# Performance work log

Measured on AMD Instinct MI355X. Metric: run time of the kernel, lower is better.

The kernel has to match this reference:

```python
import jax, jax.numpy as jnp
import numpy as np

LN_EPS = 1e-5

def _layernorm(x, scale, bias):
    mu = jnp.mean(x, axis=-1, keepdims=True)
    var = jnp.var(x, axis=-1, keepdims=True)
    return (x - mu) * jax.lax.rsqrt(var + LN_EPS) * scale + bias

def setup_inputs() -> dict:
    T, node_num, num_nodes, E, C = 4, 10000, 50000, 256, 128
    key = jax.random.key(0)
    ks = jax.random.split(key, 12)
    s = lambda fan_in: 1.0 / np.sqrt(fan_in)
    return {
        "x": jax.random.normal(ks[0], (T * node_num, E), jnp.float32),
        "batched_x": jax.random.normal(ks[1], (num_nodes, E), jnp.float32),
        "indices": jax.random.randint(ks[2], (T, node_num), 0, num_nodes, jnp.int32),
        "ln_d_scale": jnp.ones((E,), jnp.float32),
        "ln_d_bias": jnp.zeros((E,), jnp.float32),
        "W1_d": jax.random.normal(ks[3], (E, 2 * E), jnp.float32) * s(E),
        "b1_d": jnp.zeros((2 * E,), jnp.float32),
        "W2_d": jax.random.normal(ks[4], (2 * E, C), jnp.float32) * s(2 * E),
        "b2_d": jnp.zeros((C,), jnp.float32),
        "ln_u_scale": jnp.ones((C,), jnp.float32),
        "ln_u_bias": jnp.zeros((C,), jnp.float32),
        "W1_u": jax.random.normal(ks[5], (C, 2 * C), jnp.float32) * s(C),
        "b1_u": jnp.zeros((2 * C,), jnp.float32),
        "W2_u": jax.random.normal(ks[6], (2 * C, E), jnp.float32) * s(2 * C),
        "b2_u": jnp.zeros((E,), jnp.float32),
    }

def reference(x, batched_x, indices, ln_d_scale, ln_d_bias, W1_d, b1_d, W2_d, b2_d,
              ln_u_scale, ln_u_bias, W1_u, b1_u, W2_u, b2_u):
    T, node_num = indices.shape
    num_nodes, E = batched_x.shape
    xr = x.reshape(T, node_num, E)
    # _to_entire: per-step scatter-add of active-node embeddings into the full node table
    def scatter_one(xi, idx):
        return jnp.zeros((num_nodes, E), x.dtype).at[idx].add(xi)
    ta = jax.vmap(scatter_one)(xr, indices)          # [T, num_nodes, E]
    inp = ta + batched_x[None]                        # broadcast entire features
    h = _layernorm(inp, ln_d_scale, ln_d_bias)
    h = jax.nn.gelu(h @ W1_d + b1_d, approximate=False) @ W2_d + b2_d  # [T, num_nodes, C]
    # _from_entire: gather each step's active nodes back, concat, LN + MLP up
    g = jnp.take_along_axis(h, indices[..., None], axis=1)  # [T, node_num, C]
    g = g.reshape(T * node_num, -1)
    g = _layernorm(g, ln_u_scale, ln_u_bias)
    out = jax.nn.gelu(g @ W1_u + b1_u, approximate=False) @ W2_u + b2_u  # [T*node_num, E]
    return out
```

## Files before the change

kernel.cpp:

```cpp
#include <hip/hip_runtime.h>
#include <math.h>

#define T_STEPS   4
#define NODE_NUM  10000
#define NUM_NODES 50000
#define E         256
#define TWO_E     512
#define CC        128
#define TWO_C     256
#define ROWS      32

typedef short bf16x8 __attribute__((ext_vector_type(8)));
typedef float f32x4  __attribute__((ext_vector_type(4)));

#define MFMA16(a, b, c) __builtin_amdgcn_mfma_f32_16x16x32_bf16((a), (b), (c), 0, 0, 0)

static __device__ unsigned short g_wt[294912];
static __device__ int g_cnt[T_STEPS * NUM_NODES];
static __device__ int g_dup[T_STEPS * NODE_NUM];
static __device__ int g_ndup[T_STEPS];

__device__ __forceinline__ float geluf(float v) {
    float p = v * (1.5957691216057308f + 0.07135481282636226f * v * v);
    return v / (1.0f + __expf(-p));
}

__device__ __forceinline__ unsigned short f2bf(float f) {
    unsigned int u = __builtin_bit_cast(unsigned int, f);
    u += 0x7fffu + ((u >> 16) & 1u);
    return (unsigned short)(u >> 16);
}

__global__ void prep_weights(const float* __restrict__ W1d, const float* __restrict__ W2d,
                             const float* __restrict__ W1u, const float* __restrict__ W2u) {
    int i = blockIdx.x * 256 + threadIdx.x;
    if (i < T_STEPS * NUM_NODES) g_cnt[i] = 0;
    if (i < T_STEPS) g_ndup[i] = 0;
    if (i < 131072) {
        int n = i >> 8, k = i & 255;
        g_wt[i] = f2bf(W1d[(size_t)k * TWO_E + n]);
    }
    if (i < 65536) {
        int n = i >> 9, k = i & 511;
        g_wt[131072 + i] = f2bf(W2d[(size_t)k * CC + n]);
    }
    if (i < 32768) {
        int n = i >> 7, k = i & 127;
        g_wt[196608 + i] = f2bf(W1u[(size_t)k * TWO_C + n]);
    }
    if (i < 65536) {
        int n = i >> 8, k = i & 255;
        g_wt[229376 + i] = f2bf(W2u[(size_t)k * E + n]);
    }
}

__global__ void count_kernel(const int* __restrict__ indices) {
    int gr = blockIdx.x * 256 + threadIdx.x;
    if (gr < T_STEPS * NODE_NUM) {
        int t = gr / NODE_NUM;
        atomicAdd(&g_cnt[t * NUM_NODES + indices[gr]], 1);
    }
}

__global__ void compact_zero_kernel(float* __restrict__ table,
                                    const int* __restrict__ indices,
                                    int gr0, int t0, int grLim, int slab) {
    int gr = gr0 + blockIdx.x * 256 + threadIdx.x;
    if (gr >= grLim) return;
    int t = gr / NODE_NUM;
    int idx = indices[gr];
    if (g_cnt[t * NUM_NODES + idx] < 2) return;
    int pos = atomicAdd(&g_ndup[slab], 1);
    g_dup[gr0 + pos] = gr;
    float4* rp = reinterpret_cast<float4*>(&table[((size_t)(t - t0) * NUM_NODES + idx) * E]);
    float4 z = make_float4(0.f, 0.f, 0.f, 0.f);
    #pragma unroll
    for (int k = 0; k < 64; ++k) rp[k] = z;
}

__global__ void scatter_list_kernel(float* __restrict__ table,
                                    const float* __restrict__ x,
                                    const int* __restrict__ indices,
                                    int gr0, int t0, int slab) {
    int nd = g_ndup[slab];
    for (int e = blockIdx.x; e < nd; e += gridDim.x) {
        int gr = g_dup[gr0 + e];
        int t = gr / NODE_NUM;
        int idx = indices[gr];
        atomicAdd(&table[((size_t)(t - t0) * NUM_NODES + idx) * E + threadIdx.x],
                  x[(size_t)gr * E + threadIdx.x]);
    }
}

__global__ __launch_bounds__(256, 3)
void mlp_kernel(const float* __restrict__ table,
                const float* __restrict__ x,
                const float* __restrict__ batched_x,
                const int* __restrict__ indices,
                const float* __restrict__ lnd_s, const float* __restrict__ lnd_b,
                const float* __restrict__ b1d, const float* __restrict__ b2d,
                const float* __restrict__ lnu_s, const float* __restrict__ lnu_b,
                const float* __restrict__ b1u, const float* __restrict__ b2u,
                float* __restrict__ out,
                int gr0, int t0, int grLim) {
    __shared__ __align__(16) unsigned char smem[50176];
    __shared__ const float* rptr[ROWS];
    __shared__ int    ridx[ROWS];

    float*          Xf  = (float*)smem;
    unsigned short* Xs  = (unsigned short*)(smem + 33280);
    unsigned short* H1  = (unsigned short*)smem;
    float*          H2f = (float*)(smem + 33280);
    unsigned short* H2b = (unsigned short*)smem;
    unsigned short* G1  = (unsigned short*)(smem + 8704);

    const unsigned short* w1t  = g_wt;
    const unsigned short* w2t  = g_wt + 131072;
    const unsigned short* w1ut = g_wt + 196608;
    const unsigned short* w2ut = g_wt + 229376;

    const int tid = threadIdx.x;
    const int w = tid >> 6, lane = tid & 63;
    const int l16 = lane & 15, quad = lane >> 4;
    const int grb = gr0 + blockIdx.x * ROWS;

    if (tid < ROWS) {
        int gr = grb + tid;
        if (gr >= grLim) gr = grLim - 1;
        int t = gr / NODE_NUM;
        int idx = indices[gr];
        ridx[tid] = idx;
        rptr[tid] = (g_cnt[t * NUM_NODES + idx] > 1)
            ? (table + ((size_t)(t - t0) * NUM_NODES + idx) * E)
            : (x + (size_t)gr * E);
    }
    __syncthreads();

    #pragma unroll
    for (int it = 0; it < 8; ++it) {
        int v = it * 256 + tid;
        int r = v >> 6;
        int c = (v & 63) * 4;
        float4 tv = *reinterpret_cast<const float4*>(rptr[r] + c);
        float4 bv = *reinterpret_cast<const float4*>(&batched_x[(size_t)ridx[r] * E + c]);
        float4 s; s.x = tv.x + bv.x; s.y = tv.y + bv.y; s.z = tv.z + bv.z; s.w = tv.w + bv.w;
        *reinterpret_cast<float4*>(&Xf[r * 260 + c]) = s;
    }
    __syncthreads();

    {
        int row = tid >> 3, l8 = tid & 7;
        float s = 0.f, sq = 0.f;
        #pragma unroll
        for (int k = 0; k < 32; ++k) {
            float v = Xf[row * 260 + k * 8 + l8];
            s += v; sq += v * v;
        }
        s  += __shfl_xor(s, 1);  s  += __shfl_xor(s, 2);  s  += __shfl_xor(s, 4);
        sq += __shfl_xor(sq, 1); sq += __shfl_xor(sq, 2); sq += __shfl_xor(sq, 4);
        float mu = s * (1.0f / E);
        float var = sq * (1.0f / E) - mu * mu;
        float rs = rsqrtf(var + 1e-5f);
        #pragma unroll
        for (int k = 0; k < 32; ++k) {
            int c = k * 8 + l8;
            float v = (Xf[row * 260 + c] - mu) * rs * lnd_s[c] + lnd_b[c];
            Xs[row * 264 + c] = f2bf(v);
        }
    }
    __syncthreads();

    {
        bf16x8 af[2][8];
        #pragma unroll
        for (int mt = 0; mt < 2; ++mt) {
            const unsigned short* base = Xs + (l16 + 16 * mt) * 264 + quad * 8;
            #pragma unroll
            for (int ks = 0; ks < 8; ++ks)
                af[mt][ks] = *reinterpret_cast<const bf16x8*>(base + ks * 32);
        }
        bf16x8 bbuf[2][8];
        {
            const unsigned short* bp = w1t + (size_t)((w * 8) * 16 + l16) * 256 + quad * 8;
            #pragma unroll
            for (int ks = 0; ks < 8; ++ks)
                bbuf[0][ks] = *reinterpret_cast<const bf16x8*>(bp + ks * 32);
        }
        #pragma unroll
        for (int nt_ = 0; nt_ < 8; ++nt_) {
            const int cb = nt_ & 1, nb = cb ^ 1;
            if (nt_ < 7) {
                const unsigned short* bp =
                    w1t + (size_t)((w * 8 + nt_ + 1) * 16 + l16) * 256 + quad * 8;
                #pragma unroll
                for (int ks = 0; ks < 8; ++ks)
                    bbuf[nb][ks] = *reinterpret_cast<const bf16x8*>(bp + ks * 32);
            }
            int n = (w * 8 + nt_) * 16 + l16;
            f32x4 a0 = {0.f, 0.f, 0.f, 0.f}, a1 = {0.f, 0.f, 0.f, 0.f};
            #pragma unroll
            for (int ks = 0; ks < 8; ++ks) {
                a0 = MFMA16(af[0][ks], bbuf[cb][ks], a0);
                a1 = MFMA16(af[1][ks], bbuf[cb][ks], a1);
            }
            float bias = b1d[n];
            #pragma unroll
            for (int reg = 0; reg < 4; ++reg) {
                int r = quad * 4 + reg;
                H1[r * 520 + n]        = f2bf(geluf(a0[reg] + bias));
                H1[(r + 16) * 520 + n] = f2bf(geluf(a1[reg] + bias));
            }
        }
    }
    __syncthreads();

    {
        f32x4 acc2[2][2];
        #pragma unroll
        for (int i = 0; i < 2; ++i)
            #pragma unroll
            for (int j = 0; j < 2; ++j) acc2[i][j] = (f32x4){0.f, 0.f, 0.f, 0.f};
        bf16x8 afk[2][8];
        #pragma unroll
        for (int mt = 0; mt < 2; ++mt) {
            const unsigned short* base = H1 + (l16 + 16 * mt) * 520 + quad * 8;
            #pragma unroll
            for (int ks = 0; ks < 8; ++ks)
                afk[mt][ks] = *reinterpret_cast<const bf16x8*>(base + ks * 32);
        }
        bf16x8 bbuf[2][8];
        {
            const unsigned short* bp = w2t + (size_t)((w * 2) * 16 + l16) * 512 + quad * 8;
            #pragma unroll
            for (int ks = 0; ks < 8; ++ks)
                bbuf[0][ks] = *reinterpret_cast<const bf16x8*>(bp + ks * 32);
        }
        #pragma unroll
        for (int s = 0; s < 4; ++s) {
            const int nt2 = s & 1;
            const int cb = s & 1, nb = cb ^ 1;
            if (s < 3) {
                const int s1 = s + 1, kh1 = s1 >> 1, nt21 = s1 & 1;
                const unsigned short* bp =
                    w2t + (size_t)((w * 2 + nt21) * 16 + l16) * 512 + kh1 * 256 + quad * 8;
                #pragma unroll
                for (int ks = 0; ks < 8; ++ks)
                    bbuf[nb][ks] = *reinterpret_cast<const bf16x8*>(bp + ks * 32);
            }
            if (s == 2) {
                #pragma unroll
                for (int mt = 0; mt < 2; ++mt) {
                    const unsigned short* base = H1 + (l16 + 16 * mt) * 520 + 256 + quad * 8;
                    #pragma unroll
                    for (int ks = 0; ks < 8; ++ks)
                        afk[mt][ks] = *reinterpret_cast<const bf16x8*>(base + ks * 32);
                }
            }
            #pragma unroll
            for (int ks = 0; ks < 8; ++ks) {
                acc2[nt2][0] = MFMA16(afk[0][ks], bbuf[cb][ks], acc2[nt2][0]);
                acc2[nt2][1] = MFMA16(afk[1][ks], bbuf[cb][ks], acc2[nt2][1]);
            }
        }
        #pragma unroll
        for (int nt2 = 0; nt2 < 2; ++nt2) {
            int n = (w * 2 + nt2) * 16 + l16;
            float bias = b2d[n];
            #pragma unroll
            for (int mt = 0; mt < 2; ++mt)
                #pragma unroll
                for (int reg = 0; reg < 4; ++reg) {
                    int r = mt * 16 + quad * 4 + reg;
                    H2f[r * 132 + n] = acc2[nt2][mt][reg] + bias;
                }
        }
    }
    __syncthreads();

    {
        int row = tid >> 3, l8 = tid & 7;
        float s = 0.f, sq = 0.f;
        #pragma unroll
        for (int k = 0; k < 16; ++k) {
            float v = H2f[row * 132 + k * 8 + l8];
            s += v; sq += v * v;
        }
        s  += __shfl_xor(s, 1);  s  += __shfl_xor(s, 2);  s  += __shfl_xor(s, 4);
        sq += __shfl_xor(sq, 1); sq += __shfl_xor(sq, 2); sq += __shfl_xor(sq, 4);
        float mu = s * (1.0f / CC);
        float var = sq * (1.0f / CC) - mu * mu;
        float rs = rsqrtf(var + 1e-5f);
        #pragma unroll
        for (int k = 0; k < 16; ++k) {
            int c = k * 8 + l8;
            float v = (H2f[row * 132 + c] - mu) * rs * lnu_s[c] + lnu_b[c];
            H2b[row * 136 + c] = f2bf(v);
        }
    }
    __syncthreads();

    {
        bf16x8 af3[2][4];
        #pragma unroll
        for (int mt = 0; mt < 2; ++mt) {
            const unsigned short* base = H2b + (l16 + 16 * mt) * 136 + quad * 8;
            #pragma unroll
            for (int ks = 0; ks < 4; ++ks)
                af3[mt][ks] = *reinterpret_cast<const bf16x8*>(base + ks * 32);
        }
        bf16x8 bbuf[2][4];
        {
            const unsigned short* bp = w1ut + (size_t)((w * 4) * 16 + l16) * 128 + quad * 8;
            #pragma unroll
            for (int ks = 0; ks < 4; ++ks)
                bbuf[0][ks] = *reinterpret_cast<const bf16x8*>(bp + ks * 32);
        }
        #pragma unroll
        for (int nt_ = 0; nt_ < 4; ++nt_) {
            const int cb = nt_ & 1, nb = cb ^ 1;
            if (nt_ < 3) {
                const unsigned short* bp =
                    w1ut + (size_t)((w * 4 + nt_ + 1) * 16 + l16) * 128 + quad * 8;
                #pragma unroll
                for (int ks = 0; ks < 4; ++ks)
                    bbuf[nb][ks] = *reinterpret_cast<const bf16x8*>(bp + ks * 32);
            }
            int n = (w * 4 + nt_) * 16 + l16;
            f32x4 a0 = {0.f, 0.f, 0.f, 0.f}, a1 = {0.f, 0.f, 0.f, 0.f};
            #pragma unroll
            for (int ks = 0; ks < 4; ++ks) {
                a0 = MFMA16(af3[0][ks], bbuf[cb][ks], a0);
                a1 = MFMA16(af3[1][ks], bbuf[cb][ks], a1);
            }
            float bias = b1u[n];
            #pragma unroll
            for (int reg = 0; reg < 4; ++reg) {
                int r = quad * 4 + reg;
                G1[r * 264 + n]        = f2bf(geluf(a0[reg] + bias));
                G1[(r + 16) * 264 + n] = f2bf(geluf(a1[reg] + bias));
            }
        }
    }
    __syncthreads();

    {
        bf16x8 af4[2][8];
        #pragma unroll
        for (int mt = 0; mt < 2; ++mt) {
            const unsigned short* base = G1 + (l16 + 16 * mt) * 264 + quad * 8;
            #pragma unroll
            for (int ks = 0; ks < 8; ++ks)
                af4[mt][ks] = *reinterpret_cast<const bf16x8*>(base + ks * 32);
        }
        bf16x8 bbuf[2][8];
        {
            const unsigned short* bp = w2ut + (size_t)((w * 4) * 16 + l16) * 256 + quad * 8;
            #pragma unroll
            for (int ks = 0; ks < 8; ++ks)
                bbuf[0][ks] = *reinterpret_cast<const bf16x8*>(bp + ks * 32);
        }
        #pragma unroll
        for (int nt_ = 0; nt_ < 4; ++nt_) {
            const int cb = nt_ & 1, nb = cb ^ 1;
            if (nt_ < 3) {
                const unsigned short* bp =
                    w2ut + (size_t)((w * 4 + nt_ + 1) * 16 + l16) * 256 + quad * 8;
                #pragma unroll
                for (int ks = 0; ks < 8; ++ks)
                    bbuf[nb][ks] = *reinterpret_cast<const bf16x8*>(bp + ks * 32);
            }
            int n = (w * 4 + nt_) * 16 + l16;
            f32x4 a0 = {0.f, 0.f, 0.f, 0.f}, a1 = {0.f, 0.f, 0.f, 0.f};
            #pragma unroll
            for (int ks = 0; ks < 8; ++ks) {
                a0 = MFMA16(af4[0][ks], bbuf[cb][ks], a0);
                a1 = MFMA16(af4[1][ks], bbuf[cb][ks], a1);
            }
            float bias = b2u[n];
            #pragma unroll
            for (int reg = 0; reg < 4; ++reg) {
                int r = quad * 4 + reg;
                int g0 = grb + r, g1 = grb + r + 16;
                if (g0 < grLim) out[(size_t)g0 * E + n] = a0[reg] + bias;
                if (g1 < grLim) out[(size_t)g1 * E + n] = a1[reg] + bias;
            }
        }
    }
}

extern "C" void kernel_launch(void* const* d_in, const int* in_sizes, int n_in,
                              void* d_out, int out_size, void* d_ws, size_t ws_size,
                              hipStream_t stream) {
    const float* x     = (const float*)d_in[0];
    const float* bx    = (const float*)d_in[1];
    const int*   idxp  = (const int*)  d_in[2];
    const float* lnd_s = (const float*)d_in[3];
    const float* lnd_b = (const float*)d_in[4];
    const float* W1d   = (const float*)d_in[5];
    const float* b1d   = (const float*)d_in[6];
    const float* W2d   = (const float*)d_in[7];
    const float* b2d   = (const float*)d_in[8];
    const float* lnu_s = (const float*)d_in[9];
    const float* lnu_b = (const float*)d_in[10];
    const float* W1u   = (const float*)d_in[11];
    const float* b1u   = (const float*)d_in[12];
    const float* W2u   = (const float*)d_in[13];
    const float* b2u   = (const float*)d_in[14];
    float* out = (float*)d_out;
    float* table = (float*)d_ws;

    const size_t slice_bytes = (size_t)NUM_NODES * E * sizeof(float);
    int tb = (int)(ws_size / slice_bytes);
    if (tb < 1) tb = 1;
    if (tb > T_STEPS) tb = T_STEPS;

    prep_weights<<<784, 256, 0, stream>>>(W1d, W2d, W1u, W2u);
    count_kernel<<<(T_STEPS * NODE_NUM + 255) / 256, 256, 0, stream>>>(idxp);

    for (int t0 = 0; t0 < T_STEPS; t0 += tb) {
        int tcur = T_STEPS - t0 < tb ? T_STEPS - t0 : tb;
        int nrows = tcur * NODE_NUM;
        int gr0 = t0 * NODE_NUM;
        int grLim = gr0 + nrows;
        int slab = t0 / tb;
        compact_zero_kernel<<<(nrows + 255) / 256, 256, 0, stream>>>(
            table, idxp, gr0, t0, grLim, slab);
        scatter_list_kernel<<<1024, E, 0, stream>>>(table, x, idxp, gr0, t0, slab);
        mlp_kernel<<<(nrows + ROWS - 1) / ROWS, 256, 0, stream>>>(
            table, x, bx, idxp, lnd_s, lnd_b, b1d, b2d,
            lnu_s, lnu_b, b1u, b2u, out, gr0, t0, grLim);
    }
}
```

Measured before the change: 289.0 us.

## Use compact slot table for duplicate scatter and launch single pass

Replaces the per-timestep full node table with a compact slot table indexed by an atomic slot assignment for nodes hit more than once. This removes the slab loop so all timesteps run in one scatter and one MLP launch, cutting launches and tail effects. It adds an index prep kernel and zeroes a fixed MAX_SLOTS region up front, which bounds duplicates at 20000 and costs extra memset bandwidth.

```diff
diff --git a/kernel.cpp b/kernel.cpp
--- a/kernel.cpp
+++ b/kernel.cpp
@@ -9,6 +9,8 @@
 #define CC        128
 #define TWO_C     256
 #define ROWS      32
+#define NROWS_ALL (T_STEPS * NODE_NUM)
+#define MAX_SLOTS 20000
 
 typedef short bf16x8 __attribute__((ext_vector_type(8)));
 typedef float f32x4  __attribute__((ext_vector_type(4)));
@@ -17,8 +19,10 @@
 
 static __device__ unsigned short g_wt[294912];
 static __device__ int g_cnt[T_STEPS * NUM_NODES];
-static __device__ int g_dup[T_STEPS * NODE_NUM];
-static __device__ int g_ndup[T_STEPS];
+static __device__ int g_slot[T_STEPS * NUM_NODES];
+static __device__ int g_nslots;
+static __device__ int g_dup[NROWS_ALL];
+static __device__ int g_ndup0;
 
 __device__ __forceinline__ float geluf(float v) {
     float p = v * (1.5957691216057308f + 0.07135481282636226f * v * v);
@@ -31,11 +35,17 @@
     return (unsigned short)(u >> 16);
 }
 
-__global__ void prep_weights(const float* __restrict__ W1d, const float* __restrict__ W2d,
+__global__ void prep_weights(float* __restrict__ ctable,
+                             const float* __restrict__ W1d, const float* __restrict__ W2d,
                              const float* __restrict__ W1u, const float* __restrict__ W2u) {
     int i = blockIdx.x * 256 + threadIdx.x;
+    if (i == 0) { g_nslots = 0; g_ndup0 = 0; }
     if (i < T_STEPS * NUM_NODES) g_cnt[i] = 0;
-    if (i < T_STEPS) g_ndup[i] = 0;
+    {
+        float4 z = make_float4(0.f, 0.f, 0.f, 0.f);
+        float4* ct4 = reinterpret_cast<float4*>(ctable);
+        for (int j = i; j < MAX_SLOTS * E / 4; j += 200704) ct4[j] = z;
+    }
     if (i < 131072) {
         int n = i >> 8, k = i & 255;
         g_wt[i] = f2bf(W1d[(size_t)k * TWO_E + n]);
@@ -56,44 +66,40 @@
 
 __global__ void count_kernel(const int* __restrict__ indices) {
     int gr = blockIdx.x * 256 + threadIdx.x;
-    if (gr < T_STEPS * NODE_NUM) {
+    if (gr < NROWS_ALL) {
         int t = gr / NODE_NUM;
         atomicAdd(&g_cnt[t * NUM_NODES + indices[gr]], 1);
     }
 }
 
-__global__ void compact_zero_kernel(float* __restrict__ table,
-                                    const int* __restrict__ indices,
-                                    int gr0, int t0, int grLim, int slab) {
-    int gr = gr0 + blockIdx.x * 256 + threadIdx.x;
-    if (gr >= grLim) return;
-    int t = gr / NODE_NUM;
-    int idx = indices[gr];
-    if (g_cnt[t * NUM_NODES + idx] < 2) return;
-    int pos = atomicAdd(&g_ndup[slab], 1);
-    g_dup[gr0 + pos] = gr;
-    float4* rp = reinterpret_cast<float4*>(&table[((size_t)(t - t0) * NUM_NODES + idx) * E]);
-    float4 z = make_float4(0.f, 0.f, 0.f, 0.f);
-    #pragma unroll
-    for (int k = 0; k < 64; ++k) rp[k] = z;
-}
-
-__global__ void scatter_list_kernel(float* __restrict__ table,
+__global__ void index_prep_kernel(const int* __restrict__ indices) {
+    int i = blockIdx.x * 256 + threadIdx.x;
+    if (i < T_STEPS * NUM_NODES && g_cnt[i] >= 2)
+        g_slot[i] = atomicAdd(&g_nslots, 1);
+    if (i < NROWS_ALL) {
+        int t = i / NODE_NUM;
+        if (g_cnt[t * NUM_NODES + indices[i]] >= 2) {
+            int p = atomicAdd(&g_ndup0, 1);
+            g_dup[p] = i;
+        }
+    }
+}
+
+__global__ void scatter_list_kernel(float* __restrict__ ctable,
                                     const float* __restrict__ x,
-                                    const int* __restrict__ indices,
-                                    int gr0, int t0, int slab) {
-    int nd = g_ndup[slab];
+                                    const int* __restrict__ indices) {
+    int nd = g_ndup0;
     for (int e = blockIdx.x; e < nd; e += gridDim.x) {
-        int gr = g_dup[gr0 + e];
+        int gr = g_dup[e];
         int t = gr / NODE_NUM;
-        int idx = indices[gr];
-        atomicAdd(&table[((size_t)(t - t0) * NUM_NODES + idx) * E + threadIdx.x],
+        int slot = g_slot[t * NUM_NODES + indices[gr]];
+        atomicAdd(&ctable[(size_t)slot * E + threadIdx.x],
                   x[(size_t)gr * E + threadIdx.x]);
     }
 }
 
 __global__ __launch_bounds__(256, 3)
-void mlp_kernel(const float* __restrict__ table,
+void mlp_kernel(const float* __restrict__ ctable,
                 const float* __restrict__ x,
                 const float* __restrict__ batched_x,
                 const int* __restrict__ indices,
@@ -102,7 +108,7 @@
                 const float* __restrict__ lnu_s, const float* __restrict__ lnu_b,
                 const float* __restrict__ b1u, const float* __restrict__ b2u,
                 float* __restrict__ out,
-                int gr0, int t0, int grLim) {
+                int grLim) {
     __shared__ __align__(16) unsigned char smem[50176];
     __shared__ const float* rptr[ROWS];
     __shared__ int    ridx[ROWS];
@@ -122,16 +128,16 @@
     const int tid = threadIdx.x;
     const int w = tid >> 6, lane = tid & 63;
     const int l16 = lane & 15, quad = lane >> 4;
-    const int grb = gr0 + blockIdx.x * ROWS;
+    const int grb = blockIdx.x * ROWS;
 
     if (tid < ROWS) {
         int gr = grb + tid;
         if (gr >= grLim) gr = grLim - 1;
         int t = gr / NODE_NUM;
-        int idx = indices[gr];
-        ridx[tid] = idx;
-        rptr[tid] = (g_cnt[t * NUM_NODES + idx] > 1)
-            ? (table + ((size_t)(t - t0) * NUM_NODES + idx) * E)
+        int key = t * NUM_NODES + indices[gr];
+        ridx[tid] = indices[gr];
+        rptr[tid] = (g_cnt[key] > 1)
+            ? (ctable + (size_t)g_slot[key] * E)
             : (x + (size_t)gr * E);
     }
     __syncthreads();
@@ -407,27 +413,14 @@
     const float* W2u   = (const float*)d_in[13];
     const float* b2u   = (const float*)d_in[14];
     float* out = (float*)d_out;
-    float* table = (float*)d_ws;
-
-    const size_t slice_bytes = (size_t)NUM_NODES * E * sizeof(float);
-    int tb = (int)(ws_size / slice_bytes);
-    if (tb < 1) tb = 1;
-    if (tb > T_STEPS) tb = T_STEPS;
-
-    prep_weights<<<784, 256, 0, stream>>>(W1d, W2d, W1u, W2u);
-    count_kernel<<<(T_STEPS * NODE_NUM + 255) / 256, 256, 0, stream>>>(idxp);
-
-    for (int t0 = 0; t0 < T_STEPS; t0 += tb) {
-        int tcur = T_STEPS - t0 < tb ? T_STEPS - t0 : tb;
-        int nrows = tcur * NODE_NUM;
-        int gr0 = t0 * NODE_NUM;
-        int grLim = gr0 + nrows;
-        int slab = t0 / tb;
-        compact_zero_kernel<<<(nrows + 255) / 256, 256, 0, stream>>>(
-            table, idxp, gr0, t0, grLim, slab);
-        scatter_list_kernel<<<1024, E, 0, stream>>>(table, x, idxp, gr0, t0, slab);
-        mlp_kernel<<<(nrows + ROWS - 1) / ROWS, 256, 0, stream>>>(
-            table, x, bx, idxp, lnd_s, lnd_b, b1d, b2d,
-            lnu_s, lnu_b, b1u, b2u, out, gr0, t0, grLim);
-    }
-}
+    float* ctable = (float*)d_ws;
+    (void)ws_size; (void)in_sizes; (void)n_in; (void)out_size;
+
+    prep_weights<<<784, 256, 0, stream>>>(ctable, W1d, W2d, W1u, W2u);
+    count_kernel<<<(NROWS_ALL + 255) / 256, 256, 0, stream>>>(idxp);
+    index_prep_kernel<<<784, 256, 0, stream>>>(idxp);
+    scatter_list_kernel<<<1024, E, 0, stream>>>(ctable, x, idxp);
+    mlp_kernel<<<NROWS_ALL / ROWS, 256, 0, stream>>>(
+        ctable, x, bx, idxp, lnd_s, lnd_b, b1d, b2d,
+        lnu_s, lnu_b, b1u, b2u, out, NROWS_ALL);
+}
```

Result: slower. 318.0 us (+10.0%).
